# Optimization experiments

Hardware: AMD Instinct MI355X
Metric: run time of the kernel (lower is better)

Reference implementation:

```python
import jax, jax.numpy as jnp
import numpy as np

B, S, D = 2, 4096, 256
H, DH, DM = 8, 32, 1024
ROPE_BASE = 10000.0
LN_EPS = 1e-5


def _layer_norm(x, g, b):
    mu = jnp.mean(x, axis=-1, keepdims=True)
    var = jnp.mean(jnp.square(x - mu), axis=-1, keepdims=True)
    return (x - mu) * jax.lax.rsqrt(var + LN_EPS) * g + b


def _rope(x):
    # x: [b, s, h, d_head]; lucidrains interleaved-pair RoPE
    s, d = x.shape[1], x.shape[-1]
    inv_freq = 1.0 / (ROPE_BASE ** (jnp.arange(0, d, 2, dtype=jnp.float32) / d))  # [d/2]
    freqs = jnp.arange(s, dtype=jnp.float32)[:, None] * inv_freq[None, :]          # [s, d/2]
    freqs = jnp.repeat(freqs, 2, axis=-1)                                          # [s, d]
    cos = jnp.cos(freqs)[None, :, None, :]
    sin = jnp.sin(freqs)[None, :, None, :]
    x1, x2 = x[..., 0::2], x[..., 1::2]
    rot = jnp.stack((-x2, x1), axis=-1).reshape(x.shape)
    return x * cos + rot * sin


def setup_inputs() -> dict:
    key = jax.random.key(0)
    ks = jax.random.split(key, 8)
    sw = 1.0 / np.sqrt(D)
    return {
        "x": jax.random.normal(ks[0], (B, S, D), jnp.float32),
        "Wq": jax.random.normal(ks[1], (D, D), jnp.float32) * sw,
        "Wk": jax.random.normal(ks[2], (D, D), jnp.float32) * sw,
        "Wv": jax.random.normal(ks[3], (D, D), jnp.float32) * sw,
        "Wo": jax.random.normal(ks[4], (D, D), jnp.float32) * sw,
        "ln1_g": jnp.ones((D,), jnp.float32),
        "ln1_b": jnp.zeros((D,), jnp.float32),
        "ln2_g": jnp.ones((D,), jnp.float32),
        "ln2_b": jnp.zeros((D,), jnp.float32),
        "W2": jax.random.normal(ks[5], (DM, D), jnp.float32) * sw,
        "b2": jnp.zeros((DM,), jnp.float32),
        "W3": jax.random.normal(ks[6], (D, DM), jnp.float32) * (1.0 / np.sqrt(DM)),
        "b3": jnp.zeros((D,), jnp.float32),
    }


def reference(x, Wq, Wk, Wv, Wo, ln1_g, ln1_b, ln2_g, ln2_b, W2, b2, W3, b3):
    b, s, d = x.shape
    h, dh = H, DH
    xn = _layer_norm(x, ln1_g, ln1_b)
    q = (xn @ Wq.T).reshape(b, s, h, dh)
    k = (xn @ Wk.T).reshape(b, s, h, dh)
    v = (xn @ Wv.T).reshape(b, s, h, dh)
    q = _rope(q)
    k = _rope(k)
    # scores: [b, h, q, k] (full matrix, matching original implementation)
    scores = jnp.einsum('bqhd,bkhd->bhqk', q, k) / np.sqrt(dh)
    attn = jax.nn.softmax(scores, axis=-1)
    out = jnp.einsum('bhqk,bkhd->bqhd', attn, v).reshape(b, s, d)
    out = out @ Wo.T
    mlp_in = out + x
    y = _layer_norm(mlp_in, ln2_g, ln2_b)
    y = jax.nn.gelu(y @ W2.T + b2, approximate=False)
    y = y @ W3.T + b3
    return y + mlp_in
```

## Files before the change

kernel.cpp:

```cpp
#include <hip/hip_runtime.h>
#include <math.h>

#define D 256
#define S 4096
#define H 8
#define DH 32
#define DM 1024
#define NTOK 8192

typedef __attribute__((ext_vector_type(8))) short short8;
typedef __attribute__((ext_vector_type(4))) float f32x4;

#define QSCALE (0.17677669529663687f * 1.4426950408889634f)

__device__ inline unsigned short f2bf(float f) {
    union { float f; unsigned u; } v; v.f = f;
    unsigned r = v.u + 0x7fffu + ((v.u >> 16) & 1u);
    return (unsigned short)(r >> 16);
}
__device__ inline void gload16(const void* g, void* l) {
    __builtin_amdgcn_global_load_lds((const __attribute__((address_space(1))) void*)g,
                                     (__attribute__((address_space(3))) void*)l, 16, 0, 0);
}

__global__ void conv_all(const float* __restrict__ Wq, const float* __restrict__ Wk,
                         const float* __restrict__ Wv, const float* __restrict__ Wo,
                         const float* __restrict__ W2, const float* __restrict__ W3,
                         unsigned short* __restrict__ wqkv, unsigned short* __restrict__ wo_b,
                         unsigned short* __restrict__ w2_b, unsigned short* __restrict__ w3_b,
                         float* __restrict__ ct, float* __restrict__ st) {
    int i = blockIdx.x * 256 + threadIdx.x;
    if (i < 196608) {
        const float* s = (i < 65536) ? Wq : ((i < 131072) ? Wk : Wv);
        wqkv[i] = f2bf(s[i & 65535]);
    } else if (i < 262144) {
        wo_b[i - 196608] = f2bf(Wo[i - 196608]);
    } else if (i < 524288) {
        w2_b[i - 262144] = f2bf(W2[i - 262144]);
    } else if (i < 786432) {
        w3_b[i - 524288] = f2bf(W3[i - 524288]);
    } else {
        int j = i - 786432;
        int spos = j >> 4, pi = j & 15;
        float inv_freq = powf(10000.0f, -(float)(2 * pi) / 32.0f);
        float fr = (float)spos * inv_freq;
        ct[j] = cosf(fr);
        st[j] = sinf(fr);
    }
}

__global__ void ln_kernel(const float* __restrict__ x, const float* __restrict__ g,
                          const float* __restrict__ b, unsigned short* __restrict__ out) {
    __shared__ float red[8];
    int row = blockIdx.x;
    int tid = threadIdx.x;
    float v = x[(size_t)row * D + tid];
    float s = v, s2 = v * v;
    #pragma unroll
    for (int off = 32; off > 0; off >>= 1) {
        s  += __shfl_xor(s, off, 64);
        s2 += __shfl_xor(s2, off, 64);
    }
    int wave = tid >> 6;
    if ((tid & 63) == 0) { red[wave] = s; red[wave + 4] = s2; }
    __syncthreads();
    float sum   = red[0] + red[1] + red[2] + red[3];
    float sumsq = red[4] + red[5] + red[6] + red[7];
    float mu  = sum * (1.0f / D);
    float var = sumsq * (1.0f / D) - mu * mu;
    float rs  = rsqrtf(var + 1e-5f);
    out[(size_t)row * D + tid] = f2bf((v - mu) * rs * g[tid] + b[tid]);
}

__global__ __launch_bounds__(256) void gemm64(const unsigned short* __restrict__ A,
        const unsigned short* __restrict__ Bw, void* __restrict__ outp,
        unsigned short* __restrict__ vt,
        const float* __restrict__ bias, const float* __restrict__ res,
        const float* __restrict__ ct, const float* __restrict__ st,
        int N, int K, int mode) {
    __shared__ unsigned short As[2][64 * 32];
    __shared__ unsigned short Bs[2][64 * 32];
    int tid = threadIdx.x;
    int w = tid >> 6, l = tid & 63;
    int lm = l & 15, lg = l >> 4;
    int wm = (w >> 1) * 32, wn = (w & 1) * 32;
    int bm = blockIdx.x * 64, bn = blockIdx.y * 64;
    const unsigned short* Ag = A + (size_t)(bm + w * 16 + (l >> 2)) * K + ((l & 3) ^ ((l >> 3) & 3)) * 8;
    const unsigned short* Bg = Bw + (size_t)(bn + w * 16 + (l >> 2)) * K + ((l & 3) ^ ((l >> 3) & 3)) * 8;
    const int kswz = (lm >> 1) & 3;
    f32x4 acc[2][2] = {};

    gload16(Ag, &As[0][w * 512]);
    gload16(Bg, &Bs[0][w * 512]);
    #pragma unroll 2
    for (int k0 = 0; k0 < K; k0 += 32) {
        int cur = (k0 >> 5) & 1;
        __syncthreads();
        if (k0 + 32 < K) {
            gload16(Ag + k0 + 32, &As[1 - cur][w * 512]);
            gload16(Bg + k0 + 32, &Bs[1 - cur][w * 512]);
        }
        short8 af[2], bf[2];
        #pragma unroll
        for (int i = 0; i < 2; ++i) af[i] = *(const short8*)&As[cur][(wm + i * 16 + lm) * 32 + (lg ^ kswz) * 8];
        #pragma unroll
        for (int i = 0; i < 2; ++i) bf[i] = *(const short8*)&Bs[cur][(wn + i * 16 + lm) * 32 + (lg ^ kswz) * 8];
        #pragma unroll
        for (int mi = 0; mi < 2; ++mi)
            #pragma unroll
            for (int ni = 0; ni < 2; ++ni)
                acc[mi][ni] = __builtin_amdgcn_mfma_f32_16x16x32_bf16(af[mi], bf[ni], acc[mi][ni], 0, 0, 0);
    }

    if (mode == 0) {
        if (bn >= 512) {
            #pragma unroll
            for (int mi = 0; mi < 2; ++mi) {
                #pragma unroll
                for (int ni = 0; ni < 2; ++ni) {
                    int ng = bn + wn + ni * 16 + lm - 512;
                    int hh = ng >> 5, dh = ng & 31;
                    int mg0 = bm + wm + mi * 16 + lg * 4;
                    int bb = mg0 >> 12, ss = mg0 & 4095;
                    ushort4 pv;
                    pv.x = f2bf(acc[mi][ni][0]); pv.y = f2bf(acc[mi][ni][1]);
                    pv.z = f2bf(acc[mi][ni][2]); pv.w = f2bf(acc[mi][ni][3]);
                    *(ushort4*)(vt + ((size_t)((bb * 8 + hh) * 32 + dh)) * S + ss) = pv;
                }
            }
        } else {
            #pragma unroll
            for (int mi = 0; mi < 2; ++mi) {
                #pragma unroll
                for (int ni = 0; ni < 2; ++ni) {
                    int ng = bn + wn + ni * 16 + lm;
                    int pi = (ng & 31) >> 1;
                    float sgn = (ng & 1) ? 1.f : -1.f;
                    float qs  = (ng < 256) ? QSCALE : 1.f;
                    #pragma unroll
                    for (int r2 = 0; r2 < 4; ++r2) {
                        int mg = bm + wm + mi * 16 + lg * 4 + r2;
                        int spos = mg & (S - 1);
                        float vv = acc[mi][ni][r2];
                        float pv = __shfl_xor(vv, 1, 64);
                        float cs = ct[spos * 16 + pi];
                        float sn = st[spos * 16 + pi];
                        float ov = (vv * cs + sgn * pv * sn) * qs;
                        ((unsigned short*)outp)[(size_t)mg * N + ng] = f2bf(ov);
                    }
                }
            }
        }
        return;
    }
    #pragma unroll
    for (int mi = 0; mi < 2; ++mi) {
        #pragma unroll
        for (int ni = 0; ni < 2; ++ni) {
            int ng = bn + wn + ni * 16 + lm;
            #pragma unroll
            for (int r2 = 0; r2 < 4; ++r2) {
                int mg = bm + wm + mi * 16 + lg * 4 + r2;
                float v = acc[mi][ni][r2];
                size_t idx = (size_t)mg * N + ng;
                if (mode == 1) {
                    ((float*)outp)[idx] = v + res[idx];
                } else if (mode == 2) {
                    float t = v + bias[ng];
                    ((unsigned short*)outp)[idx] = f2bf(0.5f * t * (1.0f + erff(t * 0.70710678118654752f)));
                } else {
                    ((float*)outp)[idx] = v + bias[ng] + res[idx];
                }
            }
        }
    }
}

__global__ __launch_bounds__(256) void attn_kernel(const unsigned short* __restrict__ Cq,
        const unsigned short* __restrict__ vt, unsigned short* __restrict__ out) {
    __shared__ unsigned short Ks[2][64][32];
    __shared__ unsigned short Vs[2][32][64];
    __shared__ unsigned short Ones[16][64];
    int tid = threadIdx.x;
    int w = tid >> 6, l = tid & 63;
    int lm = l & 15, lg = l >> 4;
    int qt = blockIdx.x & 63;
    int bh = blockIdx.x >> 6;
    int b = bh >> 3, h = bh & 7;
    int q0 = qt * 64 + w * 16;

    {
        unsigned short val = (tid < 16) ? (unsigned short)0x3F80 : (unsigned short)0;
        *(ushort4*)(&Ones[0][0] + tid * 4) = make_ushort4(val, val, val, val);
    }

    const short8 qf = *(const short8*)(Cq + ((size_t)(b * S + q0 + lm)) * 768 + h * DH + lg * 8);
    int p = w * 16 + (l >> 2);
    int krow = ((p >> 5) << 5) + (((p >> 2) & 3) << 3) + (((p >> 4) & 1) << 2) + (p & 3);
    const unsigned short* kg = Cq + ((size_t)(b * S)) * 768 + 256 + h * 32
                               + (size_t)krow * 768 + ((l & 3) ^ ((l >> 3) & 3)) * 8;
    const unsigned short* vg = vt + ((size_t)(bh * 32 + w * 8 + (l >> 3))) * S + ((l & 7) ^ (l >> 3)) * 8;
    const int kswz = (lm >> 1) & 3;
    const int vswz = lm & 7;

    f32x4 o0 = {0.f, 0.f, 0.f, 0.f}, o1 = {0.f, 0.f, 0.f, 0.f}, o2 = {0.f, 0.f, 0.f, 0.f};
    const f32x4 z = {0.f, 0.f, 0.f, 0.f};

    gload16(kg, &Ks[0][w * 16][0]);
    gload16(vg, &Vs[0][w * 8][0]);

    #pragma unroll 2
    for (int it = 0; it < S / 64; ++it) {
        int cur = it & 1;
        __syncthreads();
        if (it + 1 < S / 64) {
            gload16(kg + (size_t)(it + 1) * 64 * 768, &Ks[1 - cur][w * 16][0]);
            gload16(vg + (size_t)(it + 1) * 64,       &Vs[1 - cur][w * 8][0]);
        }
        #pragma unroll
        for (int half = 0; half < 2; ++half) {
            short8 kf0 = *(const short8*)&Ks[cur][half * 32 + lm][(lg ^ kswz) * 8];
            short8 kf1 = *(const short8*)&Ks[cur][half * 32 + 16 + lm][(lg ^ kswz) * 8];
            f32x4 s0 = __builtin_amdgcn_mfma_f32_16x16x32_bf16(kf0, qf, z, 0, 0, 0);
            f32x4 s1 = __builtin_amdgcn_mfma_f32_16x16x32_bf16(kf1, qf, z, 0, 0, 0);
            unsigned u0[4], u1[4];
            #pragma unroll
            for (int i = 0; i < 4; ++i) {
                union { float f; unsigned u; } c0, c1;
                c0.f = __builtin_amdgcn_exp2f(s0[i]);
                c1.f = __builtin_amdgcn_exp2f(s1[i]);
                u0[i] = c0.u;
                u1[i] = c1.u;
            }
            union { unsigned u[4]; short8 s; } pk;
            pk.u[0] = __builtin_amdgcn_perm(u0[1], u0[0], 0x07060302u);
            pk.u[1] = __builtin_amdgcn_perm(u0[3], u0[2], 0x07060302u);
            pk.u[2] = __builtin_amdgcn_perm(u1[1], u1[0], 0x07060302u);
            pk.u[3] = __builtin_amdgcn_perm(u1[3], u1[2], 0x07060302u);
            short8 pf = pk.s;
            int vc = ((half * 4 + lg) ^ vswz) * 8;
            short8 va0 = *(const short8*)&Vs[cur][lm][vc];
            short8 va1 = *(const short8*)&Vs[cur][16 + lm][vc];
            short8 va2 = *(const short8*)&Ones[lm][vc];
            o0 = __builtin_amdgcn_mfma_f32_16x16x32_bf16(va0, pf, o0, 0, 0, 0);
            o1 = __builtin_amdgcn_mfma_f32_16x16x32_bf16(va1, pf, o1, 0, 0, 0);
            o2 = __builtin_amdgcn_mfma_f32_16x16x32_bf16(va2, pf, o2, 0, 0, 0);
        }
    }
    float lsum = __shfl(o2[0], lm, 64);
    float inv = 1.0f / lsum;
    ushort4 r0, r1;
    r0.x = f2bf(o0[0] * inv); r0.y = f2bf(o0[1] * inv);
    r0.z = f2bf(o0[2] * inv); r0.w = f2bf(o0[3] * inv);
    r1.x = f2bf(o1[0] * inv); r1.y = f2bf(o1[1] * inv);
    r1.z = f2bf(o1[2] * inv); r1.w = f2bf(o1[3] * inv);
    unsigned short* ob = out + ((size_t)(b * S + q0 + lm)) * D + h * DH;
    *(ushort4*)(ob + lg * 4)      = r0;
    *(ushort4*)(ob + 16 + lg * 4) = r1;
}

extern "C" void kernel_launch(void* const* d_in, const int* in_sizes, int n_in,
                              void* d_out, int out_size, void* d_ws, size_t ws_size,
                              hipStream_t stream) {
    const float* x     = (const float*)d_in[0];
    const float* Wq    = (const float*)d_in[1];
    const float* Wk    = (const float*)d_in[2];
    const float* Wv    = (const float*)d_in[3];
    const float* Wo    = (const float*)d_in[4];
    const float* ln1_g = (const float*)d_in[5];
    const float* ln1_b = (const float*)d_in[6];
    const float* ln2_g = (const float*)d_in[7];
    const float* ln2_b = (const float*)d_in[8];
    const float* W2    = (const float*)d_in[9];
    const float* b2    = (const float*)d_in[10];
    const float* W3    = (const float*)d_in[11];
    const float* b3    = (const float*)d_in[12];

    char* w8 = (char*)d_ws;
    unsigned short* wqkv = (unsigned short*)(w8);
    unsigned short* wo_b = (unsigned short*)(w8 + 393216);
    unsigned short* w2_b = (unsigned short*)(w8 + 524288);
    unsigned short* w3_b = (unsigned short*)(w8 + 1048576);
    float*          ct   = (float*)(w8 + 1572864);
    float*          st   = (float*)(w8 + 1835008);
    unsigned short* xn   = (unsigned short*)(w8 + 2097152);
    unsigned short* Cq   = (unsigned short*)(w8 + 6291456);
    unsigned short* hb   = Cq;
    unsigned short* vtb  = (unsigned short*)(w8 + 23068672);
    unsigned short* ab   = (unsigned short*)(w8 + 27262976);
    float*          mlpin= (float*)(w8 + 31457280);
    unsigned short* yn   = xn;

    conv_all<<<3328, 256, 0, stream>>>(Wq, Wk, Wv, Wo, W2, W3, wqkv, wo_b, w2_b, w3_b, ct, st);
    ln_kernel<<<NTOK, 256, 0, stream>>>(x, ln1_g, ln1_b, xn);
    gemm64<<<dim3(128, 12), 256, 0, stream>>>(xn, wqkv, Cq, vtb, nullptr, nullptr, ct, st, 768, 256, 0);
    attn_kernel<<<1024, 256, 0, stream>>>(Cq, vtb, ab);
    gemm64<<<dim3(128, 4), 256, 0, stream>>>(ab, wo_b, mlpin, nullptr, nullptr, x, nullptr, nullptr, 256, 256, 1);
    ln_kernel<<<NTOK, 256, 0, stream>>>(mlpin, ln2_g, ln2_b, yn);
    gemm64<<<dim3(128, 16), 256, 0, stream>>>(yn, w2_b, hb, nullptr, b2, nullptr, nullptr, nullptr, 1024, 256, 2);
    gemm64<<<dim3(128, 4), 256, 0, stream>>>(hb, w3_b, (float*)d_out, nullptr, b3, mlpin, nullptr, nullptr, 256, 1024, 3);
}
```

Baseline: 219.2 us.

## Enlarge GEMM M-tile to 128 and share K/V tiles across 8-wave attention blocks

The GEMM kernel now computes a 128x64 output tile per block, with each wave holding 4x2 MFMA accumulators, so every B-tile load is reused across twice as many rows and the grid is halved. The attention kernel now runs 512 threads covering 128 queries per block. Four waves load K and four load V into shared memory, which halves K/V global traffic per query. The trade-off is fewer blocks, which can lower occupancy and parallelism on a GPU with many CUs, plus higher register pressure in the GEMM.

```diff
diff --git a/kernel.cpp b/kernel.cpp
--- a/kernel.cpp
+++ b/kernel.cpp
@@ -72,25 +72,26 @@
     out[(size_t)row * D + tid] = f2bf((v - mu) * rs * g[tid] + b[tid]);
 }
 
-__global__ __launch_bounds__(256) void gemm64(const unsigned short* __restrict__ A,
+__global__ __launch_bounds__(256) void gemm128(const unsigned short* __restrict__ A,
         const unsigned short* __restrict__ Bw, void* __restrict__ outp,
         unsigned short* __restrict__ vt,
         const float* __restrict__ bias, const float* __restrict__ res,
         const float* __restrict__ ct, const float* __restrict__ st,
         int N, int K, int mode) {
-    __shared__ unsigned short As[2][64 * 32];
+    __shared__ unsigned short As[2][128 * 32];
     __shared__ unsigned short Bs[2][64 * 32];
     int tid = threadIdx.x;
     int w = tid >> 6, l = tid & 63;
     int lm = l & 15, lg = l >> 4;
-    int wm = (w >> 1) * 32, wn = (w & 1) * 32;
-    int bm = blockIdx.x * 64, bn = blockIdx.y * 64;
+    int wm = (w >> 1) * 64, wn = (w & 1) * 32;
+    int bm = blockIdx.x * 128, bn = blockIdx.y * 64;
     const unsigned short* Ag = A + (size_t)(bm + w * 16 + (l >> 2)) * K + ((l & 3) ^ ((l >> 3) & 3)) * 8;
     const unsigned short* Bg = Bw + (size_t)(bn + w * 16 + (l >> 2)) * K + ((l & 3) ^ ((l >> 3) & 3)) * 8;
     const int kswz = (lm >> 1) & 3;
-    f32x4 acc[2][2] = {};
+    f32x4 acc[4][2] = {};
 
     gload16(Ag, &As[0][w * 512]);
+    gload16(Ag + (size_t)64 * K, &As[0][2048 + w * 512]);
     gload16(Bg, &Bs[0][w * 512]);
     #pragma unroll 2
     for (int k0 = 0; k0 < K; k0 += 32) {
@@ -98,15 +99,16 @@
         __syncthreads();
         if (k0 + 32 < K) {
             gload16(Ag + k0 + 32, &As[1 - cur][w * 512]);
+            gload16(Ag + (size_t)64 * K + k0 + 32, &As[1 - cur][2048 + w * 512]);
             gload16(Bg + k0 + 32, &Bs[1 - cur][w * 512]);
         }
-        short8 af[2], bf[2];
-        #pragma unroll
-        for (int i = 0; i < 2; ++i) af[i] = *(const short8*)&As[cur][(wm + i * 16 + lm) * 32 + (lg ^ kswz) * 8];
+        short8 af[4], bf[2];
+        #pragma unroll
+        for (int i = 0; i < 4; ++i) af[i] = *(const short8*)&As[cur][(wm + i * 16 + lm) * 32 + (lg ^ kswz) * 8];
         #pragma unroll
         for (int i = 0; i < 2; ++i) bf[i] = *(const short8*)&Bs[cur][(wn + i * 16 + lm) * 32 + (lg ^ kswz) * 8];
         #pragma unroll
-        for (int mi = 0; mi < 2; ++mi)
+        for (int mi = 0; mi < 4; ++mi)
             #pragma unroll
             for (int ni = 0; ni < 2; ++ni)
                 acc[mi][ni] = __builtin_amdgcn_mfma_f32_16x16x32_bf16(af[mi], bf[ni], acc[mi][ni], 0, 0, 0);
@@ -115,7 +117,7 @@
     if (mode == 0) {
         if (bn >= 512) {
             #pragma unroll
-            for (int mi = 0; mi < 2; ++mi) {
+            for (int mi = 0; mi < 4; ++mi) {
                 #pragma unroll
                 for (int ni = 0; ni < 2; ++ni) {
                     int ng = bn + wn + ni * 16 + lm - 512;
@@ -130,7 +132,7 @@
             }
         } else {
             #pragma unroll
-            for (int mi = 0; mi < 2; ++mi) {
+            for (int mi = 0; mi < 4; ++mi) {
                 #pragma unroll
                 for (int ni = 0; ni < 2; ++ni) {
                     int ng = bn + wn + ni * 16 + lm;
@@ -154,7 +156,7 @@
         return;
     }
     #pragma unroll
-    for (int mi = 0; mi < 2; ++mi) {
+    for (int mi = 0; mi < 4; ++mi) {
         #pragma unroll
         for (int ni = 0; ni < 2; ++ni) {
             int ng = bn + wn + ni * 16 + lm;
@@ -176,7 +178,7 @@
     }
 }
 
-__global__ __launch_bounds__(256) void attn_kernel(const unsigned short* __restrict__ Cq,
+__global__ __launch_bounds__(512) void attn_kernel(const unsigned short* __restrict__ Cq,
         const unsigned short* __restrict__ vt, unsigned short* __restrict__ out) {
     __shared__ unsigned short Ks[2][64][32];
     __shared__ unsigned short Vs[2][32][64];
@@ -184,38 +186,43 @@
     int tid = threadIdx.x;
     int w = tid >> 6, l = tid & 63;
     int lm = l & 15, lg = l >> 4;
-    int qt = blockIdx.x & 63;
-    int bh = blockIdx.x >> 6;
+    int qt = blockIdx.x & 31;
+    int bh = blockIdx.x >> 5;
     int b = bh >> 3, h = bh & 7;
-    int q0 = qt * 64 + w * 16;
-
-    {
+    int q0 = qt * 128 + w * 16;
+
+    if (tid < 256) {
         unsigned short val = (tid < 16) ? (unsigned short)0x3F80 : (unsigned short)0;
         *(ushort4*)(&Ones[0][0] + tid * 4) = make_ushort4(val, val, val, val);
     }
 
     const short8 qf = *(const short8*)(Cq + ((size_t)(b * S + q0 + lm)) * 768 + h * DH + lg * 8);
-    int p = w * 16 + (l >> 2);
+    int ws = w & 3;
+    int p = ws * 16 + (l >> 2);
     int krow = ((p >> 5) << 5) + (((p >> 2) & 3) << 3) + (((p >> 4) & 1) << 2) + (p & 3);
     const unsigned short* kg = Cq + ((size_t)(b * S)) * 768 + 256 + h * 32
                                + (size_t)krow * 768 + ((l & 3) ^ ((l >> 3) & 3)) * 8;
-    const unsigned short* vg = vt + ((size_t)(bh * 32 + w * 8 + (l >> 3))) * S + ((l & 7) ^ (l >> 3)) * 8;
+    const unsigned short* vg = vt + ((size_t)(bh * 32 + ws * 8 + (l >> 3))) * S + ((l & 7) ^ (l >> 3)) * 8;
+    unsigned short* klds0 = &Ks[0][ws * 16][0];
+    unsigned short* vlds0 = &Vs[0][ws * 8][0];
+    unsigned short* klds1 = &Ks[1][ws * 16][0];
+    unsigned short* vlds1 = &Vs[1][ws * 8][0];
     const int kswz = (lm >> 1) & 3;
     const int vswz = lm & 7;
 
     f32x4 o0 = {0.f, 0.f, 0.f, 0.f}, o1 = {0.f, 0.f, 0.f, 0.f}, o2 = {0.f, 0.f, 0.f, 0.f};
     const f32x4 z = {0.f, 0.f, 0.f, 0.f};
 
-    gload16(kg, &Ks[0][w * 16][0]);
-    gload16(vg, &Vs[0][w * 8][0]);
+    if (w < 4) gload16(kg, klds0);
+    else       gload16(vg, vlds0);
 
     #pragma unroll 2
     for (int it = 0; it < S / 64; ++it) {
         int cur = it & 1;
         __syncthreads();
         if (it + 1 < S / 64) {
-            gload16(kg + (size_t)(it + 1) * 64 * 768, &Ks[1 - cur][w * 16][0]);
-            gload16(vg + (size_t)(it + 1) * 64,       &Vs[1 - cur][w * 8][0]);
+            if (w < 4) gload16(kg + (size_t)(it + 1) * 64 * 768, cur ? klds0 : klds1);
+            else       gload16(vg + (size_t)(it + 1) * 64,       cur ? vlds0 : vlds1);
         }
         #pragma unroll
         for (int half = 0; half < 2; ++half) {
@@ -293,10 +300,10 @@
 
     conv_all<<<3328, 256, 0, stream>>>(Wq, Wk, Wv, Wo, W2, W3, wqkv, wo_b, w2_b, w3_b, ct, st);
     ln_kernel<<<NTOK, 256, 0, stream>>>(x, ln1_g, ln1_b, xn);
-    gemm64<<<dim3(128, 12), 256, 0, stream>>>(xn, wqkv, Cq, vtb, nullptr, nullptr, ct, st, 768, 256, 0);
-    attn_kernel<<<1024, 256, 0, stream>>>(Cq, vtb, ab);
-    gemm64<<<dim3(128, 4), 256, 0, stream>>>(ab, wo_b, mlpin, nullptr, nullptr, x, nullptr, nullptr, 256, 256, 1);
+    gemm128<<<dim3(64, 12), 256, 0, stream>>>(xn, wqkv, Cq, vtb, nullptr, nullptr, ct, st, 768, 256, 0);
+    attn_kernel<<<512, 512, 0, stream>>>(Cq, vtb, ab);
+    gemm128<<<dim3(64, 4), 256, 0, stream>>>(ab, wo_b, mlpin, nullptr, nullptr, x, nullptr, nullptr, 256, 256, 1);
     ln_kernel<<<NTOK, 256, 0, stream>>>(mlpin, ln2_g, ln2_b, yn);
-    gemm64<<<dim3(128, 16), 256, 0, stream>>>(yn, w2_b, hb, nullptr, b2, nullptr, nullptr, nullptr, 1024, 256, 2);
-    gemm64<<<dim3(128, 4), 256, 0, stream>>>(hb, w3_b, (float*)d_out, nullptr, b3, mlpin, nullptr, nullptr, 256, 1024, 3);
-}
+    gemm128<<<dim3(64, 16), 256, 0, stream>>>(yn, w2_b, hb, nullptr, b2, nullptr, nullptr, nullptr, 1024, 256, 2);
+    gemm128<<<dim3(64, 4), 256, 0, stream>>>(hb, w3_b, (float*)d_out, nullptr, b3, mlpin, nullptr, nullptr, 256, 1024, 3);
+}
```

After: 209.6 us. -4.4%, faster.
